# Kernel tuning notes

Measured on AMD Instinct MI355X. Metric: run time of the kernel, lower is better.

The kernel has to match this reference:

```python
import jax, jax.numpy as jnp
import numpy as np

KS = 3          # kernel_size
DILS = (1, 2)   # dilation list
NH = 8          # num_heads


def _unfold(x, k, r):
    # x: [B, d, H, W] -> [B, d, k*k, H, W], matching nn.Unfold(k, dilation=r,
    # padding=r*(k-1)//2): kernel positions enumerated row-major over (kh, kw).
    B, d, H, W = x.shape
    pad = r * (k - 1) // 2
    xp = jnp.pad(x, ((0, 0), (0, 0), (pad, pad), (pad, pad)))
    patches = [xp[:, :, i * r:i * r + H, j * r:j * r + W]
               for i in range(k) for j in range(k)]
    return jnp.stack(patches, axis=2)


def setup_inputs() -> dict:
    key = jax.random.key(0)
    k1, k2, k3, k4 = jax.random.split(key, 4)
    B, H, W, C = 2, 160, 160, 128
    return {
        "x": jax.random.normal(k1, (B, H, W, C), dtype=jnp.float32),
        "qkv_w": jax.random.normal(k2, (3 * C, C), dtype=jnp.float32) * 0.05,
        "proj_w": jax.random.normal(k3, (C, C), dtype=jnp.float32) * 0.05,
        "proj_b": jax.random.normal(k4, (C,), dtype=jnp.float32) * 0.05,
    }


def reference(x, qkv_w, proj_w, proj_b):
    B, H, W, C = x.shape
    nd = len(DILS)
    hd = C // NH               # head_dim = 16
    d = C // nd                # channels per dilation group = 64
    h = d // hd                # heads per dilation group = 4
    scale = hd ** -0.5
    L = H * W

    xc = x.transpose(0, 3, 1, 2)                       # [B, C, H, W]
    qkv = jnp.einsum('bchw,oc->bohw', xc, qkv_w)       # 1x1 conv, no bias
    qkv = qkv.reshape(B, 3, nd, d, H, W)

    outs = []
    for i, r in enumerate(DILS):
        q, kk, v = qkv[:, 0, i], qkv[:, 1, i], qkv[:, 2, i]   # [B, d, H, W]
        qh = q.reshape(B, h, hd, L).transpose(0, 1, 3, 2)      # [B, h, L, hd]
        ku = _unfold(kk, KS, r).reshape(B, h, hd, KS * KS, L)  # [B, h, hd, 9, L]
        vu = _unfold(v, KS, r).reshape(B, h, hd, KS * KS, L)
        attn = jnp.einsum('bhld,bhdkl->bhlk', qh, ku) * scale  # [B, h, L, 9]
        attn = jax.nn.softmax(attn, axis=-1)
        o = jnp.einsum('bhlk,bhdkl->bhld', attn, vu)           # [B, h, L, hd]
        outs.append(o.transpose(0, 2, 1, 3).reshape(B, H, W, d))

    y = jnp.concatenate(outs, axis=-1)                  # [B, H, W, C]
    return y @ proj_w.T + proj_b
```

## Files before the change

### kernel.cpp

```cpp
#include <hip/hip_runtime.h>
#include <cstdint>

#define HW_ 160
#define NPIX (2*160*160)

typedef __attribute__((ext_vector_type(8))) short short8;
typedef __attribute__((ext_vector_type(4))) float f32x4;

__device__ __forceinline__ unsigned short f2bf(float f) {
  union { float f; unsigned u; } v; v.f = f;
  unsigned r = v.u + 0x7fffu + ((v.u >> 16) & 1u);
  return (unsigned short)(r >> 16);
}
__device__ __forceinline__ float bflo(unsigned u) {
  union { unsigned u; float f; } v; v.u = u << 16; return v.f;
}
__device__ __forceinline__ float bfhi(unsigned u) {
  union { unsigned u; float f; } v; v.u = u & 0xffff0000u; return v.f;
}

__device__ __forceinline__ short8 cvt8(const float4& x0, const float4& x1) {
  short8 h;
  h[0] = (short)f2bf(x0.x); h[1] = (short)f2bf(x0.y);
  h[2] = (short)f2bf(x0.z); h[3] = (short)f2bf(x0.w);
  h[4] = (short)f2bf(x1.x); h[5] = (short)f2bf(x1.y);
  h[6] = (short)f2bf(x1.z); h[7] = (short)f2bf(x1.w);
  return h;
}

__global__ __launch_bounds__(256)
void cvt_w(const float* __restrict__ qw, const float* __restrict__ pw,
           unsigned short* __restrict__ dst) {
  int i = (blockIdx.x * 256 + threadIdx.x) * 4;
  const float* src = (i < 49152) ? (qw + i) : (pw + (i - 49152));
  float4 v = *(const float4*)src;
  dst[i] = f2bf(v.x); dst[i + 1] = f2bf(v.y);
  dst[i + 2] = f2bf(v.z); dst[i + 3] = f2bf(v.w);
}

__global__ __launch_bounds__(256, 4)
void qkv_gemm(const float* __restrict__ x, const unsigned short* __restrict__ wq,
              unsigned int* __restrict__ qt2) {
  __shared__ short As[64 * 128];
  const int t = threadIdx.x;
  const int p0 = blockIdx.x * 64;
  const int og = blockIdx.y;

  const float* A = x + (size_t)p0 * 128;
#pragma unroll
  for (int i = 0; i < 4; ++i) {
    int f = t + i * 256;
    int row = f >> 4;
    float4 x0 = *(const float4*)(A + f * 8);
    float4 x1 = *(const float4*)(A + f * 8 + 4);
    int dst = (row * 256 + (f & 15) * 16) ^ ((row & 7) << 4);
    *(short8*)((char*)As + dst) = cvt8(x0, x1);
  }
  __syncthreads();

  const int lane = t & 63, wv = t >> 6;
  const int wp = wv & 1, wc = wv >> 1;
  const int lr = lane & 15, lk = lane >> 4;

  short8 af[2][4];
#pragma unroll
  for (int m = 0; m < 2; ++m)
#pragma unroll
    for (int kk = 0; kk < 4; ++kk) {
      int row = wp * 32 + m * 16 + lr;
      int off = (row * 256 + kk * 64 + lk * 16) ^ ((row & 7) << 4);
      af[m][kk] = *(const short8*)((const char*)As + off);
    }

#pragma unroll
  for (int it = 0; it < 3; ++it) {
    const int o0 = og * 192 + it * 64 + wc * 32;
    short8 bfr[2][4];
#pragma unroll
    for (int n = 0; n < 2; ++n) {
      const unsigned short* wr_ = wq + (size_t)(o0 + n * 16 + lr) * 128;
#pragma unroll
      for (int kk = 0; kk < 4; ++kk)
        bfr[n][kk] = *(const short8*)(wr_ + kk * 32 + lk * 8);
    }
    f32x4 acc[2][2];
#pragma unroll
    for (int n = 0; n < 2; ++n)
#pragma unroll
      for (int m = 0; m < 2; ++m) acc[n][m] = 0.f;
#pragma unroll
    for (int kk = 0; kk < 4; ++kk)
#pragma unroll
      for (int n = 0; n < 2; ++n)
#pragma unroll
        for (int m = 0; m < 2; ++m)
          acc[n][m] = __builtin_amdgcn_mfma_f32_16x16x32_bf16(
              bfr[n][kk], af[m][kk], acc[n][m], 0, 0, 0);
#pragma unroll
    for (int n = 0; n < 2; ++n)
#pragma unroll
      for (int m = 0; m < 2; ++m) {
        int ob = o0 + n * 16 + lk * 4;
        int p = p0 + wp * 32 + m * 16 + lr;
        unsigned u0 = ((unsigned)f2bf(acc[n][m][1]) << 16) | f2bf(acc[n][m][0]);
        unsigned u1 = ((unsigned)f2bf(acc[n][m][3]) << 16) | f2bf(acc[n][m][2]);
        qt2[(size_t)(ob >> 1) * NPIX + p] = u0;
        qt2[(size_t)((ob >> 1) + 1) * NPIX + p] = u1;
      }
  }
}

__global__ __launch_bounds__(256, 2)
void attn_kernel(const unsigned int* __restrict__ qt2,
                 unsigned short* __restrict__ y) {
  const int t = threadIdx.x, lane = t & 63, head = t >> 6;
  const int dil = blockIdx.y, r = dil ? 2 : 1;
  const int p = blockIdx.x * 64 + lane;
  const int rem = p % (HW_ * HW_);
  const int yy = rem / HW_;
  const int xx = rem - yy * HW_;
  const int brow2 = (dil * 64 + head * 16) >> 1;

  const unsigned int* qp = qt2 + (size_t)brow2 * NPIX + p;
  float q[16];
#pragma unroll
  for (int c2 = 0; c2 < 8; ++c2) {
    unsigned u = qp[(size_t)c2 * NPIX];
    q[2 * c2] = bflo(u); q[2 * c2 + 1] = bfhi(u);
  }

  int np[9];
  bool val[9];
#pragma unroll
  for (int jy = 0; jy < 3; ++jy)
#pragma unroll
    for (int jx = 0; jx < 3; ++jx) {
      const int j = jy * 3 + jx;
      const int dy = (jy - 1) * r, dx = (jx - 1) * r;
      val[j] = ((unsigned)(yy + dy) < HW_) && ((unsigned)(xx + dx) < HW_);
      int q_ = p + dy * HW_ + dx;
      np[j] = min(max(q_, 0), NPIX - 1);
    }

  float l[9];
#pragma unroll
  for (int j = 0; j < 9; ++j) l[j] = 0.f;
  const unsigned int* kp = qt2 + (size_t)(64 + brow2) * NPIX;
#pragma unroll
  for (int c2 = 0; c2 < 8; ++c2) {
    const unsigned int* rp = kp + (size_t)c2 * NPIX;
    const float qa = q[2 * c2], qb = q[2 * c2 + 1];
#pragma unroll
    for (int j = 0; j < 9; ++j) {
      unsigned u = rp[np[j]];
      l[j] += qa * bflo(u) + qb * bfhi(u);
    }
  }
#pragma unroll
  for (int j = 0; j < 9; ++j) l[j] = val[j] ? l[j] * 0.25f : 0.f;

  float mx = l[0];
#pragma unroll
  for (int j = 1; j < 9; ++j) mx = fmaxf(mx, l[j]);
  float e[9], s = 0.f;
#pragma unroll
  for (int j = 0; j < 9; ++j) { e[j] = __expf(l[j] - mx); s += e[j]; }
#pragma unroll
  for (int j = 0; j < 9; ++j) if (!val[j]) e[j] = 0.f;
  const float inv = 1.0f / s;

  float o[16];
#pragma unroll
  for (int c = 0; c < 16; ++c) o[c] = 0.f;
  const unsigned int* vp = qt2 + (size_t)(128 + brow2) * NPIX;
#pragma unroll
  for (int c2 = 0; c2 < 8; ++c2) {
    const unsigned int* rp = vp + (size_t)c2 * NPIX;
#pragma unroll
    for (int j = 0; j < 9; ++j) {
      unsigned u = rp[np[j]];
      o[2 * c2] += e[j] * bflo(u);
      o[2 * c2 + 1] += e[j] * bfhi(u);
    }
  }

  short8 h0, h1;
#pragma unroll
  for (int c = 0; c < 8; ++c) h0[c] = (short)f2bf(o[c] * inv);
#pragma unroll
  for (int c = 0; c < 8; ++c) h1[c] = (short)f2bf(o[c + 8] * inv);
  unsigned short* yp = y + (size_t)p * 128 + dil * 64 + head * 16;
  *(short8*)yp = h0;
  *(short8*)(yp + 8) = h1;
}

__global__ __launch_bounds__(512, 4)
void proj_gemm(const unsigned short* __restrict__ Yg,
               const unsigned short* __restrict__ wpb,
               const float* __restrict__ bias, float* __restrict__ C) {
  __shared__ short Ys[64 * 128];
  __shared__ short Ws[128 * 128];
  const int t = threadIdx.x;
  const int p0 = blockIdx.x * 64;

  const short* A = (const short*)Yg + (size_t)p0 * 128;
#pragma unroll
  for (int i = 0; i < 2; ++i) {
    int f = t + i * 512;
    int row = f >> 4;
    int dst = (row * 256 + (f & 15) * 16) ^ ((row & 7) << 4);
    *(short8*)((char*)Ys + dst) = *(const short8*)(A + f * 8);
  }
#pragma unroll
  for (int i = 0; i < 4; ++i) {
    int f = t + i * 512;
    int row = f >> 4;
    int dst = (row * 256 + (f & 15) * 16) ^ ((row & 7) << 4);
    *(short8*)((char*)Ws + dst) = *(const short8*)((const short*)wpb + f * 8);
  }
  __syncthreads();

  const int lane = t & 63, wv = t >> 6;
  const int wq_ = wv & 3, wo = wv >> 2;
  const int lr = lane & 15, lk = lane >> 4;

  short8 a[4], b[4][4];
#pragma unroll
  for (int kk = 0; kk < 4; ++kk) {
    int row = wq_ * 16 + lr;
    int off = (row * 256 + kk * 64 + lk * 16) ^ ((row & 7) << 4);
    a[kk] = *(const short8*)((const char*)Ys + off);
  }
#pragma unroll
  for (int n = 0; n < 4; ++n)
#pragma unroll
    for (int kk = 0; kk < 4; ++kk) {
      int row = wo * 64 + n * 16 + lr;
      int off = (row * 256 + kk * 64 + lk * 16) ^ ((row & 7) << 4);
      b[n][kk] = *(const short8*)((const char*)Ws + off);
    }

  f32x4 acc[4];
#pragma unroll
  for (int n = 0; n < 4; ++n) acc[n] = 0.f;
#pragma unroll
  for (int kk = 0; kk < 4; ++kk)
#pragma unroll
    for (int n = 0; n < 4; ++n)
      acc[n] = __builtin_amdgcn_mfma_f32_16x16x32_bf16(a[kk], b[n][kk], acc[n], 0, 0, 0);

#pragma unroll
  for (int n = 0; n < 4; ++n) {
    int ccol = wo * 64 + n * 16 + lr;
    float bv = bias[ccol];
    int crow = p0 + wq_ * 16 + lk * 4;
#pragma unroll
    for (int i = 0; i < 4; ++i)
      C[(size_t)(crow + i) * 128 + ccol] = acc[n][i] + bv;
  }
}

extern "C" void kernel_launch(void* const* d_in, const int* in_sizes, int n_in,
                              void* d_out, int out_size, void* d_ws, size_t ws_size,
                              hipStream_t stream) {
  const float* x      = (const float*)d_in[0];
  const float* qkv_w  = (const float*)d_in[1];
  const float* proj_w = (const float*)d_in[2];
  const float* proj_b = (const float*)d_in[3];
  float* out = (float*)d_out;

  unsigned int* qt2 = (unsigned int*)d_ws;
  unsigned short* yws = (unsigned short*)(qt2 + (size_t)192 * NPIX);
  unsigned short* wbf = yws + (size_t)NPIX * 128;
  const unsigned short* wqbf = wbf;
  const unsigned short* wpbf = wbf + 49152;

  cvt_w<<<64, 256, 0, stream>>>(qkv_w, proj_w, wbf);

  qkv_gemm<<<dim3(NPIX / 64, 2), 256, 0, stream>>>(x, wqbf, qt2);

  attn_kernel<<<dim3(NPIX / 64, 2), 256, 0, stream>>>(qt2, yws);

  proj_gemm<<<NPIX / 64, 512, 0, stream>>>(yws, wpbf, proj_b, out);
}
```

Before: 139.7 us.

## Fuse neighborhood attention with output projection via shared-memory tile

Merges the attention and projection kernels into one 512-thread block per 64 pixels. The attention result is written straight into a swizzled LDS tile, so the bf16 intermediate no longer makes a round trip through global memory. Each block now converts the fp32 projection weights to bf16 in-kernel instead of using a prepass, which adds redundant conversion work per block. B fragments are loaded per k-step to cut register pressure. Each block now handles both dilation groups, which halves the grid size.

```diff
diff --git a/kernel.cpp b/kernel.cpp
--- a/kernel.cpp
+++ b/kernel.cpp
@@ -29,11 +29,9 @@
 }
 
 __global__ __launch_bounds__(256)
-void cvt_w(const float* __restrict__ qw, const float* __restrict__ pw,
-           unsigned short* __restrict__ dst) {
+void cvt_w(const float* __restrict__ qw, unsigned short* __restrict__ dst) {
   int i = (blockIdx.x * 256 + threadIdx.x) * 4;
-  const float* src = (i < 49152) ? (qw + i) : (pw + (i - 49152));
-  float4 v = *(const float4*)src;
+  float4 v = *(const float4*)(qw + i);
   dst[i] = f2bf(v.x); dst[i + 1] = f2bf(v.y);
   dst[i + 2] = f2bf(v.z); dst[i + 3] = f2bf(v.w);
 }
@@ -110,12 +108,29 @@
   }
 }
 
-__global__ __launch_bounds__(256, 2)
-void attn_kernel(const unsigned int* __restrict__ qt2,
-                 unsigned short* __restrict__ y) {
-  const int t = threadIdx.x, lane = t & 63, head = t >> 6;
-  const int dil = blockIdx.y, r = dil ? 2 : 1;
-  const int p = blockIdx.x * 64 + lane;
+__global__ __launch_bounds__(512, 4)
+void attn_proj(const unsigned int* __restrict__ qt2,
+               const float* __restrict__ wp_f32,
+               const float* __restrict__ bias, float* __restrict__ C) {
+  __shared__ short Ys[64 * 128];
+  __shared__ short Ws[128 * 128];
+  const int t = threadIdx.x;
+  const int p0 = blockIdx.x * 64;
+
+#pragma unroll
+  for (int i = 0; i < 4; ++i) {
+    int f = t + i * 512;
+    int row = f >> 4;
+    float4 x0 = *(const float4*)(wp_f32 + f * 8);
+    float4 x1 = *(const float4*)(wp_f32 + f * 8 + 4);
+    int dst = (row * 256 + (f & 15) * 16) ^ ((row & 7) << 4);
+    *(short8*)((char*)Ws + dst) = cvt8(x0, x1);
+  }
+
+  const int lane = t & 63, wv = t >> 6;
+  const int dil = wv >> 2, head = wv & 3;
+  const int r = dil ? 2 : 1;
+  const int p = p0 + lane;
   const int rem = p % (HW_ * HW_);
   const int yy = rem / HW_;
   const int xx = rem - yy * HW_;
@@ -184,70 +199,47 @@
     }
   }
 
-  short8 h0, h1;
-#pragma unroll
-  for (int c = 0; c < 8; ++c) h0[c] = (short)f2bf(o[c] * inv);
-#pragma unroll
-  for (int c = 0; c < 8; ++c) h1[c] = (short)f2bf(o[c + 8] * inv);
-  unsigned short* yp = y + (size_t)p * 128 + dil * 64 + head * 16;
-  *(short8*)yp = h0;
-  *(short8*)(yp + 8) = h1;
-}
-
-__global__ __launch_bounds__(512, 4)
-void proj_gemm(const unsigned short* __restrict__ Yg,
-               const unsigned short* __restrict__ wpb,
-               const float* __restrict__ bias, float* __restrict__ C) {
-  __shared__ short Ys[64 * 128];
-  __shared__ short Ws[128 * 128];
-  const int t = threadIdx.x;
-  const int p0 = blockIdx.x * 64;
-
-  const short* A = (const short*)Yg + (size_t)p0 * 128;
-#pragma unroll
-  for (int i = 0; i < 2; ++i) {
-    int f = t + i * 512;
-    int row = f >> 4;
-    int dst = (row * 256 + (f & 15) * 16) ^ ((row & 7) << 4);
-    *(short8*)((char*)Ys + dst) = *(const short8*)(A + f * 8);
-  }
-#pragma unroll
-  for (int i = 0; i < 4; ++i) {
-    int f = t + i * 512;
-    int row = f >> 4;
-    int dst = (row * 256 + (f & 15) * 16) ^ ((row & 7) << 4);
-    *(short8*)((char*)Ws + dst) = *(const short8*)((const short*)wpb + f * 8);
+  {
+    short8 h0, h1;
+#pragma unroll
+    for (int c = 0; c < 8; ++c) h0[c] = (short)f2bf(o[c] * inv);
+#pragma unroll
+    for (int c = 0; c < 8; ++c) h1[c] = (short)f2bf(o[c + 8] * inv);
+    int colb = (dil * 64 + head * 16) * 2;
+    int base = (lane * 256 + colb) ^ ((lane & 7) << 4);
+    *(short8*)((char*)Ys + base) = h0;
+    int base2 = (lane * 256 + colb + 16) ^ ((lane & 7) << 4);
+    *(short8*)((char*)Ys + base2) = h1;
   }
   __syncthreads();
 
-  const int lane = t & 63, wv = t >> 6;
   const int wq_ = wv & 3, wo = wv >> 2;
   const int lr = lane & 15, lk = lane >> 4;
 
-  short8 a[4], b[4][4];
+  short8 a[4];
 #pragma unroll
   for (int kk = 0; kk < 4; ++kk) {
     int row = wq_ * 16 + lr;
     int off = (row * 256 + kk * 64 + lk * 16) ^ ((row & 7) << 4);
     a[kk] = *(const short8*)((const char*)Ys + off);
   }
-#pragma unroll
-  for (int n = 0; n < 4; ++n)
-#pragma unroll
-    for (int kk = 0; kk < 4; ++kk) {
+
+  f32x4 acc[4];
+#pragma unroll
+  for (int n = 0; n < 4; ++n) acc[n] = 0.f;
+#pragma unroll
+  for (int kk = 0; kk < 4; ++kk) {
+    short8 b[4];
+#pragma unroll
+    for (int n = 0; n < 4; ++n) {
       int row = wo * 64 + n * 16 + lr;
       int off = (row * 256 + kk * 64 + lk * 16) ^ ((row & 7) << 4);
-      b[n][kk] = *(const short8*)((const char*)Ws + off);
-    }
-
-  f32x4 acc[4];
-#pragma unroll
-  for (int n = 0; n < 4; ++n) acc[n] = 0.f;
-#pragma unroll
-  for (int kk = 0; kk < 4; ++kk)
+      b[n] = *(const short8*)((const char*)Ws + off);
+    }
 #pragma unroll
     for (int n = 0; n < 4; ++n)
-      acc[n] = __builtin_amdgcn_mfma_f32_16x16x32_bf16(a[kk], b[n][kk], acc[n], 0, 0, 0);
+      acc[n] = __builtin_amdgcn_mfma_f32_16x16x32_bf16(a[kk], b[n], acc[n], 0, 0, 0);
+  }
 
 #pragma unroll
   for (int n = 0; n < 4; ++n) {
@@ -270,16 +262,11 @@
   float* out = (float*)d_out;
 
   unsigned int* qt2 = (unsigned int*)d_ws;
-  unsigned short* yws = (unsigned short*)(qt2 + (size_t)192 * NPIX);
-  unsigned short* wbf = yws + (size_t)NPIX * 128;
-  const unsigned short* wqbf = wbf;
-  const unsigned short* wpbf = wbf + 49152;
-
-  cvt_w<<<64, 256, 0, stream>>>(qkv_w, proj_w, wbf);
+  unsigned short* wqbf = (unsigned short*)(qt2 + (size_t)192 * NPIX);
+
+  cvt_w<<<48, 256, 0, stream>>>(qkv_w, wqbf);
 
   qkv_gemm<<<dim3(NPIX / 64, 2), 256, 0, stream>>>(x, wqbf, qt2);
 
-  attn_kernel<<<dim3(NPIX / 64, 2), 256, 0, stream>>>(qt2, yws);
-
-  proj_gemm<<<NPIX / 64, 512, 0, stream>>>(yws, wpbf, proj_b, out);
-}
+  attn_proj<<<NPIX / 64, 512, 0, stream>>>(qt2, proj_w, proj_b, out);
+}
```

New measurement: 137.6 us. Within noise of the previous version (-1.5%).
